# Performance work log

Hardware: AMD Instinct MI355X
Metric: run time of the kernel (lower is better)

The kernel has to match this reference:

```python
import jax, jax.numpy as jnp
import numpy as np

DN = ('NCDHW', 'OIDHW', 'NCDHW')

def conv3d(x, w, b):
    # kernel 3, padding 1, stride 1 -> SAME
    y = jax.lax.conv_general_dilated(x, w, window_strides=(1, 1, 1), padding='SAME', dimension_numbers=DN)
    return y + b[None, :, None, None, None]

def setup_inputs() -> dict:
    key = jax.random.key(0)
    ks = jax.random.split(key, 7)
    C, Cqk = 64, 8  # in_channels, in_channels // 8
    x = jax.random.normal(ks[0], (2, C, 20, 20, 20), dtype=jnp.float32)
    fan_qk = C * 27
    fan_v = C * 27
    wq = jax.random.normal(ks[1], (Cqk, C, 3, 3, 3), dtype=jnp.float32) / np.sqrt(fan_qk)
    bq = jax.random.normal(ks[2], (Cqk,), dtype=jnp.float32) * 0.01
    wk = jax.random.normal(ks[3], (Cqk, C, 3, 3, 3), dtype=jnp.float32) / np.sqrt(fan_qk)
    bk = jax.random.normal(ks[4], (Cqk,), dtype=jnp.float32) * 0.01
    wv = jax.random.normal(ks[5], (C, C, 3, 3, 3), dtype=jnp.float32) / np.sqrt(fan_v)
    bv = jax.random.normal(ks[6], (C,), dtype=jnp.float32) * 0.01
    return {'x': x, 'wq': wq, 'bq': bq, 'wk': wk, 'bk': bk, 'wv': wv, 'bv': bv}

def reference(x, wq, bq, wk, bk, wv, bv):
    b, C, h, w, d = x.shape
    n = h * w * d
    M = conv3d(x, wq, bq).reshape(b, -1, n)   # (b, C/8, n)
    N = conv3d(x, wk, bk).reshape(b, -1, n)   # (b, C/8, n)
    V = conv3d(x, wv, bv).reshape(b, C, n)    # (b, C, n)
    # B[b,i,j] = softmax_j( sum_c M[b,c,i] * N[b,c,j] )  (no scale factor, as in source)
    scores = jnp.einsum('bci,bcj->bij', M, N)
    B = jax.nn.softmax(scores, axis=-1)
    # GSA[b,c,i] = sum_j V[b,c,j] * B[b,i,j]
    out = jnp.einsum('bcj,bij->bci', V, B).reshape(b, C, h, w, d)
    return out
```

## Files before the change

### kernel.cpp

```cpp
#include <hip/hip_runtime.h>
#include <hip/hip_bf16.h>
#include <math.h>

#define NSP 8000
#define CIN 64
#define LOG2E 1.4426950408889634f

typedef __attribute__((ext_vector_type(8)))  short    bf16x8;
typedef __attribute__((ext_vector_type(4)))  float    f32x4;
typedef __attribute__((ext_vector_type(16))) float    f32x16;
typedef __attribute__((ext_vector_type(8)))  _Float16 f16x8;
typedef __attribute__((ext_vector_type(2)))  __fp16   fp16x2;

__device__ __forceinline__ ushort f2bf(float f) {
    unsigned u = __float_as_uint(f);
    unsigned r = (u + 0x7fffu + ((u >> 16) & 1u)) >> 16;
    return (ushort)r;
}

__global__ __launch_bounds__(256) void wconv_kernel(
    const float* __restrict__ wq, const float* __restrict__ wk,
    const float* __restrict__ wv, ushort* __restrict__ wbf)
{
    const int ci   = blockIdx.y;
    const int idx2 = blockIdx.x * 256 + threadIdx.x;
    const int co   = idx2 >> 5;
    const int kk   = idx2 & 31;
    float v = 0.0f;
    if (kk < 27) {
        if (co < 8)       v = wq[(co * 64 + ci) * 27 + kk];
        else if (co < 16) v = wk[((co - 8) * 64 + ci) * 27 + kk];
        else              v = wv[((co - 16) * 64 + ci) * 27 + kk];
    }
    wbf[ci * 2560 + idx2] = f2bf(v);
}

__global__ __launch_bounds__(256) void conv_mfma_kernel(
    const float* __restrict__ x, const ushort* __restrict__ wbf,
    const float* __restrict__ bq, const float* __restrict__ bk,
    const float* __restrict__ bv,
    _Float16* __restrict__ Qt, _Float16* __restrict__ Kt, _Float16* __restrict__ Vg)
{
    const int t = threadIdx.x;
    const int l = t & 63;
    const int w = t >> 6;
    const int b = blockIdx.y;
    const int s = blockIdx.x * 16 + (l & 15);
    const int klo = (l >> 4) * 8;

    const int z  = s / 400;
    const int r0 = s - z * 400;
    const int y  = r0 / 20;
    const int xx = r0 - y * 20;

    int   pos[8];
    float wt[8];
    #pragma unroll
    for (int e = 0; e < 8; ++e) {
        const int tap = klo + e;
        bool ok = false; int p = 0;
        if (tap < 27) {
            const int dz = tap / 9, dy = (tap / 3) % 3, dx = tap % 3;
            const int zz = z + dz - 1, yy = y + dy - 1, xq = xx + dx - 1;
            ok = ((unsigned)zz < 20u) && ((unsigned)yy < 20u) && ((unsigned)xq < 20u);
            p  = ok ? (zz * 400 + yy * 20 + xq) : 0;
        }
        pos[e] = p;
        wt[e]  = ok ? 1.0f : 0.0f;
    }

    const float*  xb = x + (size_t)b * CIN * NSP;
    const ushort* wl = wbf + (l & 15) * 32 + klo;
    const int c0 = w * 16;

    f32x4 acc[5];
    #pragma unroll
    for (int ct = 0; ct < 5; ++ct) acc[ct] = (f32x4)0.0f;

    float  g[8];
    bf16x8 a[5];

    #define GATHER(CI, G) { const float* xp = xb + (CI) * NSP;            \
        _Pragma("unroll") for (int e = 0; e < 8; ++e) G[e] = xp[pos[e]] * wt[e]; }
    #define LOADA(CI, A) { const ushort* wp = wl + (CI) * 2560;           \
        _Pragma("unroll") for (int ct = 0; ct < 5; ++ct)                  \
            A[ct] = *(const bf16x8*)(wp + ct * 512); }
    #define CONSUME(G, A) { bf16x8 bfrag;                                 \
        _Pragma("unroll") for (int e = 0; e < 8; ++e) bfrag[e] = (short)f2bf(G[e]); \
        _Pragma("unroll") for (int ct = 0; ct < 5; ++ct)                  \
            acc[ct] = __builtin_amdgcn_mfma_f32_16x16x32_bf16(A[ct], bfrag, acc[ct], 0, 0, 0); }

    GATHER(c0, g); LOADA(c0, a);
    for (int ci = c0; ci < c0 + 15; ++ci) {
        float  gn[8];
        bf16x8 an[5];
        GATHER(ci + 1, gn); LOADA(ci + 1, an);
        CONSUME(g, a);
        #pragma unroll
        for (int e = 0; e < 8; ++e) g[e] = gn[e];
        #pragma unroll
        for (int ct = 0; ct < 5; ++ct) a[ct] = an[ct];
    }
    CONSUME(g, a);
    #undef GATHER
    #undef LOADA
    #undef CONSUME

    __shared__ float lacc[3][64][20];
    if (w > 0) {
        #pragma unroll
        for (int ct = 0; ct < 5; ++ct)
            *(f32x4*)&lacc[w - 1][l][ct * 4] = acc[ct];
    }
    __syncthreads();
    if (w == 0) {
        #pragma unroll
        for (int ct = 0; ct < 5; ++ct) {
            #pragma unroll
            for (int r = 0; r < 4; ++r) {
                float v = acc[ct][r] + lacc[0][l][ct * 4 + r]
                        + lacc[1][l][ct * 4 + r] + lacc[2][l][ct * 4 + r];
                const int co = ct * 16 + (l >> 4) * 4 + r;
                if (co < 8)
                    Qt[((size_t)b * NSP + s) * 8 + co] = (_Float16)((v + bq[co]) * LOG2E);
                else if (co < 16)
                    Kt[((size_t)b * NSP + s) * 8 + (co - 8)] = (_Float16)(v + bk[co - 8]);
                else
                    Vg[((size_t)b * 64 + co - 16) * NSP + s] = (_Float16)(v + bv[co - 16]);
            }
        }
    }
}

__global__ __launch_bounds__(512, 4) void attn_kernel(
    const _Float16* __restrict__ Qt, const _Float16* __restrict__ Kt,
    const _Float16* __restrict__ Vg, float* __restrict__ out)
{
    const int t  = threadIdx.x;
    const int l  = t & 63;
    const int w  = t >> 6;
    const int b  = blockIdx.y;
    const int i0 = blockIdx.x * 32;
    const int il = l & 31;
    const int hi = l >> 5;

    const _Float16* Qtb = Qt + (size_t)b * NSP * 8;
    const _Float16* Ktb = Kt + (size_t)b * NSP * 8;
    const _Float16* Vb  = Vg + (size_t)b * 64 * NSP;

    __shared__ __align__(16) char smem[34816];
    _Float16* p_base = (_Float16*)smem;
    float*    mrg    = (float*)smem;
    float*    mml    = (float*)(smem + 32768);
    float*    lsm    = (float*)(smem + 33792);

    _Float16* pw = p_base + w * 1152;

    f16x8 qf = (f16x8)(_Float16)0.0f;
    if (l < 32) qf = *(const f16x8*)&Qtb[(size_t)(i0 + il) * 8];

    float m = -INFINITY, lsum = 0.0f;
    f32x16 acc0 = (f32x16)0.0f, acc1 = (f32x16)0.0f;
    const f32x16 zero16 = (f32x16)0.0f;

    for (int jt = w; jt < 250; jt += 8) {
        const int j0 = jt * 32;

        f16x8 kf = (f16x8)(_Float16)0.0f;
        if (l < 32) kf = *(const f16x8*)&Ktb[(size_t)(j0 + il) * 8];

        f16x8 vf0k0 = *(const f16x8*)&Vb[(size_t)(il)      * NSP + j0 + 8 * hi];
        f16x8 vf0k1 = *(const f16x8*)&Vb[(size_t)(il)      * NSP + j0 + 16 + 8 * hi];
        f16x8 vf1k0 = *(const f16x8*)&Vb[(size_t)(32 + il) * NSP + j0 + 8 * hi];
        f16x8 vf1k1 = *(const f16x8*)&Vb[(size_t)(32 + il) * NSP + j0 + 16 + 8 * hi];

        f32x16 sacc = __builtin_amdgcn_mfma_f32_32x32x16_f16(kf, qf, zero16, 0, 0, 0);

        float pm = sacc[0];
        #pragma unroll
        for (int r = 1; r < 16; ++r) pm = fmaxf(pm, sacc[r]);
        pm = fmaxf(pm, __shfl_xor(pm, 32));

        if (__any(pm > m + 8.0f)) {
            const float mn = fmaxf(m, pm);
            const float sc = __builtin_amdgcn_exp2f(m - mn);
            #pragma unroll
            for (int r = 0; r < 16; ++r) { acc0[r] *= sc; acc1[r] *= sc; }
            lsum *= sc;
            m = mn;
        }

        float ps = 0.0f;
        float pr[16];
        #pragma unroll
        for (int r = 0; r < 16; ++r) {
            pr[r] = __builtin_amdgcn_exp2f(sacc[r] - m);
            ps += pr[r];
        }
        ps += __shfl_xor(ps, 32);
        lsum += ps;

        #pragma unroll
        for (int g = 0; g < 4; ++g) {
            union { fp16x2 h[2]; uint2 u; } pk;
            pk.h[0] = __builtin_amdgcn_cvt_pkrtz(pr[g * 4 + 0], pr[g * 4 + 1]);
            pk.h[1] = __builtin_amdgcn_cvt_pkrtz(pr[g * 4 + 2], pr[g * 4 + 3]);
            *(uint2*)(pw + il * 36 + g * 8 + hi * 4) = pk.u;
        }
        asm volatile("s_waitcnt lgkmcnt(0)" ::: "memory");
        __builtin_amdgcn_sched_barrier(0);

        {
            const f16x8 pf0 = *(const f16x8*)(pw + il * 36 + 8 * hi);
            acc0 = __builtin_amdgcn_mfma_f32_32x32x16_f16(vf0k0, pf0, acc0, 0, 0, 0);
            acc1 = __builtin_amdgcn_mfma_f32_32x32x16_f16(vf1k0, pf0, acc1, 0, 0, 0);
            const f16x8 pf1 = *(const f16x8*)(pw + il * 36 + 16 + 8 * hi);
            acc0 = __builtin_amdgcn_mfma_f32_32x32x16_f16(vf0k1, pf1, acc0, 0, 0, 0);
            acc1 = __builtin_amdgcn_mfma_f32_32x32x16_f16(vf1k1, pf1, acc1, 0, 0, 0);
        }
    }

    __syncthreads();
    if (l < 32) mml[w * 32 + il] = m;
    __syncthreads();
    float gm = mml[il];
    #pragma unroll
    for (int ww = 1; ww < 8; ++ww) gm = fmaxf(gm, mml[ww * 32 + il]);
    const float f = __builtin_amdgcn_exp2f(m - gm);
    if (l < 32) lsm[w * 32 + il] = lsum * f;
    #pragma unroll
    for (int r = 0; r < 16; ++r) { acc0[r] *= f; acc1[r] *= f; }

    float* ob = out + (size_t)b * 64 * NSP + i0;

    #pragma unroll
    for (int r = 0; r < 16; ++r) {
        const int cl = (r & 3) + 8 * (r >> 2) + 4 * hi;
        mrg[w * 1024 + cl * 32 + il] = acc0[r];
    }
    __syncthreads();
    #pragma unroll
    for (int rep = 0; rep < 2; ++rep) {
        const int e = t + rep * 512;
        const int c = e >> 5, i = e & 31;
        float s = 0.0f, lg = 0.0f;
        #pragma unroll
        for (int ww = 0; ww < 8; ++ww) {
            s  += mrg[ww * 1024 + c * 32 + i];
            lg += lsm[ww * 32 + i];
        }
        ob[(size_t)c * NSP + i] = s / lg;
    }
    __syncthreads();

    #pragma unroll
    for (int r = 0; r < 16; ++r) {
        const int cl = (r & 3) + 8 * (r >> 2) + 4 * hi;
        mrg[w * 1024 + cl * 32 + il] = acc1[r];
    }
    __syncthreads();
    #pragma unroll
    for (int rep = 0; rep < 2; ++rep) {
        const int e = t + rep * 512;
        const int c = e >> 5, i = e & 31;
        float s = 0.0f, lg = 0.0f;
        #pragma unroll
        for (int ww = 0; ww < 8; ++ww) {
            s  += mrg[ww * 1024 + c * 32 + i];
            lg += lsm[ww * 32 + i];
        }
        ob[(size_t)(32 + c) * NSP + i] = s / lg;
    }
}

extern "C" void kernel_launch(void* const* d_in, const int* in_sizes, int n_in,
                              void* d_out, int out_size, void* d_ws, size_t ws_size,
                              hipStream_t stream) {
    const float* x  = (const float*)d_in[0];
    const float* wq = (const float*)d_in[1];
    const float* bq = (const float*)d_in[2];
    const float* wk = (const float*)d_in[3];
    const float* bk = (const float*)d_in[4];
    const float* wv = (const float*)d_in[5];
    const float* bv = (const float*)d_in[6];
    float* out = (float*)d_out;

    ushort*   wbf = (ushort*)d_ws;
    _Float16* Qt  = (_Float16*)((char*)d_ws + 327680);
    _Float16* Kt  = (_Float16*)((char*)d_ws + 583680);
    _Float16* Vg  = (_Float16*)((char*)d_ws + 839680);

    wconv_kernel<<<dim3(10, 64), 256, 0, stream>>>(wq, wk, wv, wbf);
    conv_mfma_kernel<<<dim3(500, 2), 256, 0, stream>>>(x, wbf, bq, bk, bv, Qt, Kt, Vg);
    attn_kernel<<<dim3(250, 2), 512, 0, stream>>>(Qt, Kt, Vg, out);
}
```

Measured before the change: 162.3 us.

## Restructure conv as padded channel-last implicit GEMM and prefetch tiled V in attention

Adds a pre-pass that converts x into a zero-padded, channel-last bf16 volume and reorders weights per tap. The conv kernel then does an implicit GEMM over taps with contiguous vector loads, with no per-element gather or masking, using one wave per block instead of four waves plus an LDS reduction. V is stored in 16-column tiles so attention loads are contiguous. Attention software-prefetches the next K/V tile, raises wave priority around the MFMAs, and replaces the final divide with a hardware reciprocal. The cost is an extra kernel launch, a larger padded workspace, and slightly less precise normalization.

After: 166.5 us. 1.03x slower.

```diff
diff --git a/kernel.cpp b/kernel.cpp
--- a/kernel.cpp
+++ b/kernel.cpp
@@ -18,115 +18,97 @@
     return (ushort)r;
 }
 
-__global__ __launch_bounds__(256) void wconv_kernel(
+__global__ __launch_bounds__(64) void wtap_kernel(
     const float* __restrict__ wq, const float* __restrict__ wk,
-    const float* __restrict__ wv, ushort* __restrict__ wbf)
+    const float* __restrict__ wv, ushort* __restrict__ wtap)
 {
-    const int ci   = blockIdx.y;
-    const int idx2 = blockIdx.x * 256 + threadIdx.x;
-    const int co   = idx2 >> 5;
-    const int kk   = idx2 & 31;
-    float v = 0.0f;
-    if (kk < 27) {
-        if (co < 8)       v = wq[(co * 64 + ci) * 27 + kk];
-        else if (co < 16) v = wk[((co - 8) * 64 + ci) * 27 + kk];
-        else              v = wv[((co - 16) * 64 + ci) * 27 + kk];
-    }
-    wbf[ci * 2560 + idx2] = f2bf(v);
-}
-
-__global__ __launch_bounds__(256) void conv_mfma_kernel(
-    const float* __restrict__ x, const ushort* __restrict__ wbf,
+    const int tap = blockIdx.x;
+    const int co  = blockIdx.y;
+    const int ci  = threadIdx.x;
+    float v;
+    if (co < 8)       v = wq[(co * 64 + ci) * 27 + tap];
+    else if (co < 16) v = wk[((co - 8) * 64 + ci) * 27 + tap];
+    else              v = wv[((co - 16) * 64 + ci) * 27 + tap];
+    wtap[((size_t)tap * 80 + co) * 64 + ci] = f2bf(v);
+}
+
+__global__ __launch_bounds__(64) void xpad_kernel(
+    const float* __restrict__ x, ushort* __restrict__ xpad)
+{
+    const int bx  = blockIdx.x;
+    const int b   = bx / 484;
+    const int rem = bx % 484;
+    const int zp  = rem / 22, yp = rem % 22;
+    const int ci  = threadIdx.x;
+    const bool zy = (zp >= 1 && zp <= 20) && (yp >= 1 && yp <= 20);
+    const float* xb = x + ((size_t)b * 64 + ci) * NSP + (zp - 1) * 400 + (yp - 1) * 20;
+    ushort* op = xpad + (size_t)b * 681472 + (size_t)(zp * 484 + yp * 22) * 64 + ci;
+    for (int xp = 0; xp < 22; ++xp) {
+        float v = 0.0f;
+        if (zy && xp >= 1 && xp <= 20) v = xb[xp - 1];
+        op[xp * 64] = f2bf(v);
+    }
+}
+
+__global__ __launch_bounds__(64, 4) void conv_mfma_kernel(
+    const ushort* __restrict__ xpad, const ushort* __restrict__ wtap,
     const float* __restrict__ bq, const float* __restrict__ bk,
     const float* __restrict__ bv,
-    _Float16* __restrict__ Qt, _Float16* __restrict__ Kt, _Float16* __restrict__ Vg)
+    _Float16* __restrict__ Qt, _Float16* __restrict__ Kt, _Float16* __restrict__ VT)
 {
-    const int t = threadIdx.x;
-    const int l = t & 63;
-    const int w = t >> 6;
-    const int b = blockIdx.y;
-    const int s = blockIdx.x * 16 + (l & 15);
-    const int klo = (l >> 4) * 8;
-
+    const int l  = threadIdx.x;
+    const int bx = blockIdx.x;
+    const int b  = blockIdx.y;
+    const int s  = bx * 16 + (l & 15);
     const int z  = s / 400;
-    const int r0 = s - z * 400;
+    const int r0 = s % 400;
     const int y  = r0 / 20;
-    const int xx = r0 - y * 20;
-
-    int   pos[8];
-    float wt[8];
-    #pragma unroll
-    for (int e = 0; e < 8; ++e) {
-        const int tap = klo + e;
-        bool ok = false; int p = 0;
-        if (tap < 27) {
-            const int dz = tap / 9, dy = (tap / 3) % 3, dx = tap % 3;
-            const int zz = z + dz - 1, yy = y + dy - 1, xq = xx + dx - 1;
-            ok = ((unsigned)zz < 20u) && ((unsigned)yy < 20u) && ((unsigned)xq < 20u);
-            p  = ok ? (zz * 400 + yy * 20 + xq) : 0;
-        }
-        pos[e] = p;
-        wt[e]  = ok ? 1.0f : 0.0f;
-    }
-
-    const float*  xb = x + (size_t)b * CIN * NSP;
-    const ushort* wl = wbf + (l & 15) * 32 + klo;
-    const int c0 = w * 16;
+    const int xx = r0 % 20;
+    const int kq = (l >> 4) * 8;
+
+    const ushort* xb = xpad + (size_t)b * 681472
+                     + (size_t)(z * 484 + y * 22 + xx) * 64 + kq;
+    const ushort* wl = wtap + (l & 15) * 64 + kq;
 
     f32x4 acc[5];
     #pragma unroll
     for (int ct = 0; ct < 5; ++ct) acc[ct] = (f32x4)0.0f;
 
-    float  g[8];
-    bf16x8 a[5];
-
-    #define GATHER(CI, G) { const float* xp = xb + (CI) * NSP;            \
-        _Pragma("unroll") for (int e = 0; e < 8; ++e) G[e] = xp[pos[e]] * wt[e]; }
-    #define LOADA(CI, A) { const ushort* wp = wl + (CI) * 2560;           \
-        _Pragma("unroll") for (int ct = 0; ct < 5; ++ct)                  \
-            A[ct] = *(const bf16x8*)(wp + ct * 512); }
-    #define CONSUME(G, A) { bf16x8 bfrag;                                 \
-        _Pragma("unroll") for (int e = 0; e < 8; ++e) bfrag[e] = (short)f2bf(G[e]); \
-        _Pragma("unroll") for (int ct = 0; ct < 5; ++ct)                  \
-            acc[ct] = __builtin_amdgcn_mfma_f32_16x16x32_bf16(A[ct], bfrag, acc[ct], 0, 0, 0); }
-
-    GATHER(c0, g); LOADA(c0, a);
-    for (int ci = c0; ci < c0 + 15; ++ci) {
-        float  gn[8];
-        bf16x8 an[5];
-        GATHER(ci + 1, gn); LOADA(ci + 1, an);
-        CONSUME(g, a);
-        #pragma unroll
-        for (int e = 0; e < 8; ++e) g[e] = gn[e];
-        #pragma unroll
-        for (int ct = 0; ct < 5; ++ct) a[ct] = an[ct];
-    }
-    CONSUME(g, a);
-    #undef GATHER
-    #undef LOADA
-    #undef CONSUME
-
-    __shared__ float lacc[3][64][20];
-    if (w > 0) {
-        #pragma unroll
-        for (int ct = 0; ct < 5; ++ct)
-            *(f32x4*)&lacc[w - 1][l][ct * 4] = acc[ct];
-    }
-    __syncthreads();
-    if (w == 0) {
-        #pragma unroll
-        for (int ct = 0; ct < 5; ++ct) {
+    for (int dz = 0; dz < 3; ++dz) {
+        for (int dy = 0; dy < 3; ++dy) {
+            const ushort* xrow = xb + (size_t)(dz * 484 + dy * 22) * 64;
+            const ushort* wrow = wl + (size_t)((dz * 3 + dy) * 3) * 80 * 64;
             #pragma unroll
-            for (int r = 0; r < 4; ++r) {
-                float v = acc[ct][r] + lacc[0][l][ct * 4 + r]
-                        + lacc[1][l][ct * 4 + r] + lacc[2][l][ct * 4 + r];
-                const int co = ct * 16 + (l >> 4) * 4 + r;
-                if (co < 8)
-                    Qt[((size_t)b * NSP + s) * 8 + co] = (_Float16)((v + bq[co]) * LOG2E);
-                else if (co < 16)
-                    Kt[((size_t)b * NSP + s) * 8 + (co - 8)] = (_Float16)(v + bk[co - 8]);
-                else
-                    Vg[((size_t)b * 64 + co - 16) * NSP + s] = (_Float16)(v + bv[co - 16]);
+            for (int dx = 0; dx < 3; ++dx) {
+                const ushort* xp2 = xrow + dx * 64;
+                const bf16x8 b0 = *(const bf16x8*)(xp2);
+                const bf16x8 b1 = *(const bf16x8*)(xp2 + 32);
+                const ushort* wp = wrow + (size_t)dx * 80 * 64;
+                #pragma unroll
+                for (int ct = 0; ct < 5; ++ct) {
+                    const bf16x8 a0 = *(const bf16x8*)(wp + ct * 16 * 64);
+                    const bf16x8 a1 = *(const bf16x8*)(wp + ct * 16 * 64 + 32);
+                    acc[ct] = __builtin_amdgcn_mfma_f32_16x16x32_bf16(a0, b0, acc[ct], 0, 0, 0);
+                    acc[ct] = __builtin_amdgcn_mfma_f32_16x16x32_bf16(a1, b1, acc[ct], 0, 0, 0);
+                }
+            }
+        }
+    }
+
+    #pragma unroll
+    for (int ct = 0; ct < 5; ++ct) {
+        #pragma unroll
+        for (int r = 0; r < 4; ++r) {
+            const int co = ct * 16 + (l >> 4) * 4 + r;
+            const float v = acc[ct][r];
+            if (co < 8)
+                Qt[((size_t)b * NSP + s) * 8 + co] = (_Float16)((v + bq[co]) * LOG2E);
+            else if (co < 16)
+                Kt[((size_t)b * NSP + s) * 8 + (co - 8)] = (_Float16)(v + bk[co - 8]);
+            else {
+                const int c = co - 16;
+                VT[(size_t)b * 512000 + ((size_t)bx * 64 + c) * 16 + (l & 15)] =
+                    (_Float16)(v + bv[c]);
             }
         }
     }
@@ -134,7 +116,7 @@
 
 __global__ __launch_bounds__(512, 4) void attn_kernel(
     const _Float16* __restrict__ Qt, const _Float16* __restrict__ Kt,
-    const _Float16* __restrict__ Vg, float* __restrict__ out)
+    const _Float16* __restrict__ VT, float* __restrict__ out)
 {
     const int t  = threadIdx.x;
     const int l  = t & 63;
@@ -146,7 +128,7 @@
 
     const _Float16* Qtb = Qt + (size_t)b * NSP * 8;
     const _Float16* Ktb = Kt + (size_t)b * NSP * 8;
-    const _Float16* Vb  = Vg + (size_t)b * 64 * NSP;
+    const _Float16* VTb = VT + (size_t)b * 512000;
 
     __shared__ __align__(16) char smem[34816];
     _Float16* p_base = (_Float16*)smem;
@@ -163,16 +145,24 @@
     f32x16 acc0 = (f32x16)0.0f, acc1 = (f32x16)0.0f;
     const f32x16 zero16 = (f32x16)0.0f;
 
-    for (int jt = w; jt < 250; jt += 8) {
-        const int j0 = jt * 32;
-
-        f16x8 kf = (f16x8)(_Float16)0.0f;
-        if (l < 32) kf = *(const f16x8*)&Ktb[(size_t)(j0 + il) * 8];
-
-        f16x8 vf0k0 = *(const f16x8*)&Vb[(size_t)(il)      * NSP + j0 + 8 * hi];
-        f16x8 vf0k1 = *(const f16x8*)&Vb[(size_t)(il)      * NSP + j0 + 16 + 8 * hi];
-        f16x8 vf1k0 = *(const f16x8*)&Vb[(size_t)(32 + il) * NSP + j0 + 8 * hi];
-        f16x8 vf1k1 = *(const f16x8*)&Vb[(size_t)(32 + il) * NSP + j0 + 16 + 8 * hi];
+#define LOADK(JT, KF) { KF = (f16x8)(_Float16)0.0f;                         \
+        if (l < 32) KF = *(const f16x8*)&Ktb[(size_t)((JT) * 32 + il) * 8]; }
+#define LOADV(JT, VF) { const int jb = (JT) * 2;                            \
+        VF##00 = *(const f16x8*)&VTb[((size_t)(jb + 0) * 64 + il) * 16 + 8 * hi];      \
+        VF##01 = *(const f16x8*)&VTb[((size_t)(jb + 1) * 64 + il) * 16 + 8 * hi];      \
+        VF##10 = *(const f16x8*)&VTb[((size_t)(jb + 0) * 64 + 32 + il) * 16 + 8 * hi]; \
+        VF##11 = *(const f16x8*)&VTb[((size_t)(jb + 1) * 64 + 32 + il) * 16 + 8 * hi]; }
+
+    int jt = w;
+    f16x8 kf, vf00, vf01, vf10, vf11;
+    LOADK(jt, kf);
+    LOADV(jt, vf);
+
+    while (jt < 250) {
+        const int jn = jt + 8;
+        const bool has = (jn < 250);
+        f16x8 kf_n, vn00, vn01, vn10, vn11;
+        if (has) { LOADK(jn, kf_n); LOADV(jn, vn); }
 
         f32x16 sacc = __builtin_amdgcn_mfma_f32_32x32x16_f16(kf, qf, zero16, 0, 0, 0);
 
@@ -191,11 +181,11 @@
         }
 
         float ps = 0.0f;
-        float pr[16];
         #pragma unroll
         for (int r = 0; r < 16; ++r) {
-            pr[r] = __builtin_amdgcn_exp2f(sacc[r] - m);
-            ps += pr[r];
+            const float p = __builtin_amdgcn_exp2f(sacc[r] - m);
+            sacc[r] = p;
+            ps += p;
         }
         ps += __shfl_xor(ps, 32);
         lsum += ps;
@@ -203,22 +193,32 @@
         #pragma unroll
         for (int g = 0; g < 4; ++g) {
             union { fp16x2 h[2]; uint2 u; } pk;
-            pk.h[0] = __builtin_amdgcn_cvt_pkrtz(pr[g * 4 + 0], pr[g * 4 + 1]);
-            pk.h[1] = __builtin_amdgcn_cvt_pkrtz(pr[g * 4 + 2], pr[g * 4 + 3]);
+            pk.h[0] = __builtin_amdgcn_cvt_pkrtz(sacc[g * 4 + 0], sacc[g * 4 + 1]);
+            pk.h[1] = __builtin_amdgcn_cvt_pkrtz(sacc[g * 4 + 2], sacc[g * 4 + 3]);
             *(uint2*)(pw + il * 36 + g * 8 + hi * 4) = pk.u;
         }
         asm volatile("s_waitcnt lgkmcnt(0)" ::: "memory");
         __builtin_amdgcn_sched_barrier(0);
 
+        __builtin_amdgcn_s_setprio(1);
         {
             const f16x8 pf0 = *(const f16x8*)(pw + il * 36 + 8 * hi);
-            acc0 = __builtin_amdgcn_mfma_f32_32x32x16_f16(vf0k0, pf0, acc0, 0, 0, 0);
-            acc1 = __builtin_amdgcn_mfma_f32_32x32x16_f16(vf1k0, pf0, acc1, 0, 0, 0);
+            acc0 = __builtin_amdgcn_mfma_f32_32x32x16_f16(vf00, pf0, acc0, 0, 0, 0);
+            acc1 = __builtin_amdgcn_mfma_f32_32x32x16_f16(vf10, pf0, acc1, 0, 0, 0);
             const f16x8 pf1 = *(const f16x8*)(pw + il * 36 + 16 + 8 * hi);
-            acc0 = __builtin_amdgcn_mfma_f32_32x32x16_f16(vf0k1, pf1, acc0, 0, 0, 0);
-            acc1 = __builtin_amdgcn_mfma_f32_32x32x16_f16(vf1k1, pf1, acc1, 0, 0, 0);
-        }
-    }
+            acc0 = __builtin_amdgcn_mfma_f32_32x32x16_f16(vf01, pf1, acc0, 0, 0, 0);
+            acc1 = __builtin_amdgcn_mfma_f32_32x32x16_f16(vf11, pf1, acc1, 0, 0, 0);
+        }
+        __builtin_amdgcn_s_setprio(0);
+
+        if (has) {
+            kf = kf_n;
+            vf00 = vn00; vf01 = vn01; vf10 = vn10; vf11 = vn11;
+        }
+        jt = jn;
+    }
+#undef LOADK
+#undef LOADV
 
     __syncthreads();
     if (l < 32) mml[w * 32 + il] = m;
@@ -243,13 +243,15 @@
     for (int rep = 0; rep < 2; ++rep) {
         const int e = t + rep * 512;
         const int c = e >> 5, i = e & 31;
-        float s = 0.0f, lg = 0.0f;
+        float sv = 0.0f, lg = 0.0f;
         #pragma unroll
         for (int ww = 0; ww < 8; ++ww) {
-            s  += mrg[ww * 1024 + c * 32 + i];
+            sv += mrg[ww * 1024 + c * 32 + i];
             lg += lsm[ww * 32 + i];
         }
-        ob[(size_t)c * NSP + i] = s / lg;
+        float inv;
+        asm("v_rcp_f32 %0, %1" : "=v"(inv) : "v"(lg));
+        ob[(size_t)c * NSP + i] = sv * inv;
     }
     __syncthreads();
 
@@ -263,13 +265,15 @@
     for (int rep = 0; rep < 2; ++rep) {
         const int e = t + rep * 512;
         const int c = e >> 5, i = e & 31;
-        float s = 0.0f, lg = 0.0f;
+        float sv = 0.0f, lg = 0.0f;
         #pragma unroll
         for (int ww = 0; ww < 8; ++ww) {
-            s  += mrg[ww * 1024 + c * 32 + i];
+            sv += mrg[ww * 1024 + c * 32 + i];
             lg += lsm[ww * 32 + i];
         }
-        ob[(size_t)(32 + c) * NSP + i] = s / lg;
+        float inv;
+        asm("v_rcp_f32 %0, %1" : "=v"(inv) : "v"(lg));
+        ob[(size_t)(32 + c) * NSP + i] = sv * inv;
     }
 }
 
@@ -285,12 +289,14 @@
     const float* bv = (const float*)d_in[6];
     float* out = (float*)d_out;
 
-    ushort*   wbf = (ushort*)d_ws;
-    _Float16* Qt  = (_Float16*)((char*)d_ws + 327680);
-    _Float16* Kt  = (_Float16*)((char*)d_ws + 583680);
-    _Float16* Vg  = (_Float16*)((char*)d_ws + 839680);
-
-    wconv_kernel<<<dim3(10, 64), 256, 0, stream>>>(wq, wk, wv, wbf);
-    conv_mfma_kernel<<<dim3(500, 2), 256, 0, stream>>>(x, wbf, bq, bk, bv, Qt, Kt, Vg);
-    attn_kernel<<<dim3(250, 2), 512, 0, stream>>>(Qt, Kt, Vg, out);
-}
+    ushort*   wtap = (ushort*)d_ws;
+    ushort*   xpad = (ushort*)((char*)d_ws + 278528);
+    _Float16* Qt   = (_Float16*)((char*)d_ws + 3004416);
+    _Float16* Kt   = (_Float16*)((char*)d_ws + 3260416);
+    _Float16* VT   = (_Float16*)((char*)d_ws + 3516416);
+
+    wtap_kernel<<<dim3(27, 80), 64, 0, stream>>>(wq, wk, wv, wtap);
+    xpad_kernel<<<dim3(968), 64, 0, stream>>>(x, xpad);
+    conv_mfma_kernel<<<dim3(500, 2), 64, 0, stream>>>(xpad, wtap, bq, bk, bv, Qt, Kt, VT);
+    attn_kernel<<<dim3(250, 2), 512, 0, stream>>>(Qt, Kt, VT, out);
+}
```
